# Kernel tuning notes

Hardware: AMD Instinct MI355X
Metric: run time of the kernel (lower is better)

The kernel has to match this reference:

```python
import jax, jax.numpy as jnp
import numpy as np

L, D, H, FF = 6, 768, 12, 3072
DH = D // H
EPS = 1e-12

def _layer_norm(x, g, b):
    mu = jnp.mean(x, axis=-1, keepdims=True)
    var = jnp.mean((x - mu) ** 2, axis=-1, keepdims=True)
    return (x - mu) * jax.lax.rsqrt(var + EPS) * g + b

def setup_inputs() -> dict:
    key = jax.random.key(0)
    ks = jax.random.split(key, 12)
    s = 0.02
    inp = {
        "x": jax.random.normal(ks[0], (8, 512, D), dtype=jnp.float32),
        "attn_mask": jnp.ones((8, 512), dtype=jnp.int32),
        "Wq": jax.random.normal(ks[1], (L, D, D), dtype=jnp.float32) * s,
        "bq": jnp.zeros((L, D), dtype=jnp.float32),
        "Wk": jax.random.normal(ks[2], (L, D, D), dtype=jnp.float32) * s,
        "bk": jnp.zeros((L, D), dtype=jnp.float32),
        "Wv": jax.random.normal(ks[3], (L, D, D), dtype=jnp.float32) * s,
        "bv": jnp.zeros((L, D), dtype=jnp.float32),
        "Wo": jax.random.normal(ks[4], (L, D, D), dtype=jnp.float32) * s,
        "bo": jnp.zeros((L, D), dtype=jnp.float32),
        "ln1_g": jnp.ones((L, D), dtype=jnp.float32),
        "ln1_b": jnp.zeros((L, D), dtype=jnp.float32),
        "W1": jax.random.normal(ks[5], (L, D, FF), dtype=jnp.float32) * s,
        "b1": jnp.zeros((L, FF), dtype=jnp.float32),
        "W2": jax.random.normal(ks[6], (L, FF, D), dtype=jnp.float32) * s,
        "b2": jnp.zeros((L, D), dtype=jnp.float32),
        "ln2_g": jnp.ones((L, D), dtype=jnp.float32),
        "ln2_b": jnp.zeros((L, D), dtype=jnp.float32),
    }
    return inp

def reference(x, attn_mask, Wq, bq, Wk, bk, Wv, bv, Wo, bo,
              ln1_g, ln1_b, W1, b1, W2, b2, ln2_g, ln2_b):
    bs, S, _ = x.shape
    mask_neg = (attn_mask == 0)[:, None, None, :]  # (bs,1,1,S)
    h = x
    for i in range(L):
        def split_heads(t):
            return t.reshape(bs, S, H, DH).transpose(0, 2, 1, 3)  # (bs,H,S,dh)
        q = split_heads(h @ Wq[i] + bq[i]) / jnp.sqrt(jnp.float32(DH))
        k = split_heads(h @ Wk[i] + bk[i])
        v = split_heads(h @ Wv[i] + bv[i])
        scores = jnp.einsum('bhqd,bhkd->bhqk', q, k)
        scores = jnp.where(mask_neg, jnp.float32(-1e9), scores)
        w = jax.nn.softmax(scores, axis=-1)
        ctx = jnp.einsum('bhqk,bhkd->bhqd', w, v)
        ctx = ctx.transpose(0, 2, 1, 3).reshape(bs, S, D)
        sa = ctx @ Wo[i] + bo[i]
        h2 = _layer_norm(sa + h, ln1_g[i], ln1_b[i])
        ffn = jax.nn.gelu(h2 @ W1[i] + b1[i], approximate=False) @ W2[i] + b2[i]
        h = _layer_norm(ffn + h2, ln2_g[i], ln2_b[i])
    return h
```

## Files before the change

kernel.cpp:

```cpp
#include <hip/hip_runtime.h>
#include <math.h>

#define NLAYER 6
#define DMODEL 768
#define NHEAD 12
#define DHEAD 64
#define FFDIM 3072
#define SEQ 512
#define BATCH 8
#define NTOK (BATCH * SEQ)
#define ND ((size_t)NTOK * DMODEL)

typedef __bf16 bf16_t;
typedef __bf16 bf16x8 __attribute__((ext_vector_type(8)));
typedef float f32x4 __attribute__((ext_vector_type(4)));

__device__ __forceinline__ float bf2f(ushort u) {
    return __uint_as_float(((unsigned int)u) << 16);
}
union BFU { __bf16 h; ushort u; };
__device__ __forceinline__ ushort f2b(float x) { BFU c; c.h = (__bf16)x; return c.u; }

#define GLDS(gp, lp) __builtin_amdgcn_global_load_lds( \
    (const __attribute__((address_space(1))) void*)(gp), \
    (__attribute__((address_space(3))) void*)(lp), 16, 0, 0)

__global__ __launch_bounds__(256) void gemm_mfma(
    const ushort* __restrict__ A, const ushort* __restrict__ Bt,
    const float* __restrict__ bias, float* __restrict__ Cf,
    ushort* __restrict__ Cb, int M, int K, int N, int act)
{
    __shared__ __align__(16) ushort As[8192];
    __shared__ __align__(16) ushort Bs[8192];

    const int t = threadIdx.x;
    const int w = t >> 6, l = t & 63;
    const int wr = w >> 1, wc = w & 1;
    const int row0 = blockIdx.y * 128, col0 = blockIdx.x * 128;

    f32x4 acc[4][4];
#pragma unroll
    for (int mi = 0; mi < 4; ++mi)
#pragma unroll
        for (int ni = 0; ni < 4; ++ni)
#pragma unroll
            for (int e = 0; e < 4; ++e) acc[mi][ni][e] = 0.f;

    const int c0 = t,       r0 = c0 >> 2, kg0 = (c0 & 3) ^ ((r0 >> 1) & 3);
    const int c1 = t + 256, r1 = c1 >> 2, kg1 = (c1 & 3) ^ ((r1 >> 1) & 3);
    const ushort* gA0 = A + (size_t)(row0 + r0) * K + kg0 * 8;
    const ushort* gA1 = A + (size_t)(row0 + r1) * K + kg1 * 8;
    const ushort* gB0 = Bt + (size_t)(col0 + r0) * K + kg0 * 8;
    const ushort* gB1 = Bt + (size_t)(col0 + r1) * K + kg1 * 8;

    const int lm = l & 15, lq = l >> 4;
    int aoff[4], boff[4];
#pragma unroll
    for (int mi = 0; mi < 4; ++mi) {
        int m = wr * 64 + mi * 16 + lm;
        aoff[mi] = m * 32 + (lq ^ ((m >> 1) & 3)) * 8;
    }
#pragma unroll
    for (int ni = 0; ni < 4; ++ni) {
        int n = wc * 64 + ni * 16 + lm;
        boff[ni] = n * 32 + (lq ^ ((n >> 1) & 3)) * 8;
    }

#define STAGE_FF(b, k0) do {                                  \
        GLDS(gA0 + (k0), &As[(b) * 4096 + w * 512]);          \
        GLDS(gA1 + (k0), &As[(b) * 4096 + 2048 + w * 512]);   \
        GLDS(gB0 + (k0), &Bs[(b) * 4096 + w * 512]);          \
        GLDS(gB1 + (k0), &Bs[(b) * 4096 + 2048 + w * 512]);   \
    } while (0)

#define COMPUTE_FF(b) do {                                                  \
        bf16x8 af[4], bfr[4];                                               \
        _Pragma("unroll")                                                   \
        for (int mi = 0; mi < 4; ++mi)                                      \
            af[mi] = *(const bf16x8*)&As[(b) * 4096 + aoff[mi]];            \
        _Pragma("unroll")                                                   \
        for (int ni = 0; ni < 4; ++ni)                                      \
            bfr[ni] = *(const bf16x8*)&Bs[(b) * 4096 + boff[ni]];           \
        _Pragma("unroll")                                                   \
        for (int mi = 0; mi < 4; ++mi)                                      \
            _Pragma("unroll")                                               \
            for (int ni = 0; ni < 4; ++ni)                                  \
                acc[mi][ni] = __builtin_amdgcn_mfma_f32_16x16x32_bf16(      \
                    af[mi], bfr[ni], acc[mi][ni], 0, 0, 0);                 \
    } while (0)

    const int nsteps = K >> 5;
    STAGE_FF(0, 0);
    __syncthreads();
    int cur = 0;
    for (int s = 0; s < nsteps - 1; ++s) {
        STAGE_FF(cur ^ 1, (s + 1) * 32);
        COMPUTE_FF(cur);
        __syncthreads();
        cur ^= 1;
    }
    COMPUTE_FF(cur);

#pragma unroll
    for (int mi = 0; mi < 4; ++mi) {
        int rowb = row0 + wr * 64 + mi * 16 + lq * 4;
#pragma unroll
        for (int ni = 0; ni < 4; ++ni) {
            int col = col0 + wc * 64 + ni * 16 + lm;
            float bv = bias[col];
#pragma unroll
            for (int r = 0; r < 4; ++r) {
                float v = acc[mi][ni][r] + bv;
                if (act == 1) v = 0.5f * v * (1.0f + erff(v * 0.70710678118654752f));
                size_t idx = (size_t)(rowb + r) * N + col;
                if (Cb) ((bf16_t*)Cb)[idx] = (bf16_t)v;
                else    Cf[idx] = v;
            }
        }
    }
#undef STAGE_FF
#undef COMPUTE_FF
}

__global__ __launch_bounds__(256) void gemm_mfma_sk(
    const ushort* __restrict__ A, const ushort* __restrict__ Bt,
    const float* __restrict__ bias, float* __restrict__ P0,
    float* __restrict__ P1, int M, int K, int N, int kLen)
{
    __shared__ __align__(16) ushort As[4096];
    __shared__ __align__(16) ushort Bs[8192];

    const int t = threadIdx.x;
    const int w = t >> 6, l = t & 63;
    const int wr = w >> 1, wc = w & 1;
    const int row0 = blockIdx.y * 64, col0 = blockIdx.x * 128;
    const int z = blockIdx.z;
    const int kOff = z * kLen;
    float* Pz = (z == 0) ? P0 : P1;

    f32x4 acc[2][4];
#pragma unroll
    for (int mi = 0; mi < 2; ++mi)
#pragma unroll
        for (int ni = 0; ni < 4; ++ni)
#pragma unroll
            for (int e = 0; e < 4; ++e) acc[mi][ni][e] = 0.f;

    const int rS = t >> 2, kg = (t & 3) ^ ((rS >> 1) & 3);
    const ushort* gA  = A  + (size_t)(row0 + rS) * K + kg * 8;
    const ushort* gB0 = Bt + (size_t)(col0 + rS) * K + kg * 8;
    const ushort* gB1 = Bt + (size_t)(col0 + 64 + rS) * K + kg * 8;

    const int lm = l & 15, lq = l >> 4;
    int aoff[2], boff[4];
#pragma unroll
    for (int mi = 0; mi < 2; ++mi) {
        int m = wr * 32 + mi * 16 + lm;
        aoff[mi] = m * 32 + (lq ^ ((m >> 1) & 3)) * 8;
    }
#pragma unroll
    for (int ni = 0; ni < 4; ++ni) {
        int n = wc * 64 + ni * 16 + lm;
        boff[ni] = n * 32 + (lq ^ ((n >> 1) & 3)) * 8;
    }

#define STAGE_SK(b, k0) do {                                  \
        GLDS(gA  + (k0), &As[(b) * 2048 + w * 512]);          \
        GLDS(gB0 + (k0), &Bs[(b) * 4096 + w * 512]);          \
        GLDS(gB1 + (k0), &Bs[(b) * 4096 + 2048 + w * 512]);   \
    } while (0)

#define COMPUTE_SK(b) do {                                                  \
        bf16x8 af[2], bfr[4];                                               \
        _Pragma("unroll")                                                   \
        for (int mi = 0; mi < 2; ++mi)                                      \
            af[mi] = *(const bf16x8*)&As[(b) * 2048 + aoff[mi]];            \
        _Pragma("unroll")                                                   \
        for (int ni = 0; ni < 4; ++ni)                                      \
            bfr[ni] = *(const bf16x8*)&Bs[(b) * 4096 + boff[ni]];           \
        _Pragma("unroll")                                                   \
        for (int mi = 0; mi < 2; ++mi)                                      \
            _Pragma("unroll")                                               \
            for (int ni = 0; ni < 4; ++ni)                                  \
                acc[mi][ni] = __builtin_amdgcn_mfma_f32_16x16x32_bf16(      \
                    af[mi], bfr[ni], acc[mi][ni], 0, 0, 0);                 \
    } while (0)

    const int nsteps = kLen >> 5;
    STAGE_SK(0, kOff);
    __syncthreads();
    int cur = 0;
    for (int s = 0; s < nsteps - 1; ++s) {
        STAGE_SK(cur ^ 1, kOff + (s + 1) * 32);
        COMPUTE_SK(cur);
        __syncthreads();
        cur ^= 1;
    }
    COMPUTE_SK(cur);

#pragma unroll
    for (int mi = 0; mi < 2; ++mi) {
        int rowb = row0 + wr * 32 + mi * 16 + lq * 4;
#pragma unroll
        for (int ni = 0; ni < 4; ++ni) {
            int col = col0 + wc * 64 + ni * 16 + lm;
            float bv = (z == 0) ? bias[col] : 0.f;
#pragma unroll
            for (int r = 0; r < 4; ++r)
                Pz[(size_t)(rowb + r) * N + col] = acc[mi][ni][r] + bv;
        }
    }
#undef STAGE_SK
#undef COMPUTE_SK
}

__global__ __launch_bounds__(256) void gemm_qkv(
    const ushort* __restrict__ A, const ushort* __restrict__ Bt,
    const float* __restrict__ bq, const float* __restrict__ bk,
    const float* __restrict__ bv,
    ushort* __restrict__ qb, ushort* __restrict__ kb, ushort* __restrict__ vtb)
{
    __shared__ __align__(16) ushort As[4096];
    __shared__ __align__(16) ushort Bs[8192];

    const int K = DMODEL;
    const int t = threadIdx.x;
    const int w = t >> 6, l = t & 63;
    const int wr = w >> 1, wc = w & 1;
    const int row0 = blockIdx.y * 64, col0 = blockIdx.x * 128;
    const int seg = blockIdx.x / 6;

    f32x4 acc[2][4];
#pragma unroll
    for (int mi = 0; mi < 2; ++mi)
#pragma unroll
        for (int ni = 0; ni < 4; ++ni)
#pragma unroll
            for (int e = 0; e < 4; ++e) acc[mi][ni][e] = 0.f;

    const int rS = t >> 2, kg = (t & 3) ^ ((rS >> 1) & 3);
    const ushort* gA  = A  + (size_t)(row0 + rS) * K + kg * 8;
    const ushort* gB0 = Bt + (size_t)(col0 + rS) * K + kg * 8;
    const ushort* gB1 = Bt + (size_t)(col0 + 64 + rS) * K + kg * 8;

    const int lm = l & 15, lq = l >> 4;
    int aoff[2], boff[4];
#pragma unroll
    for (int mi = 0; mi < 2; ++mi) {
        int m = wr * 32 + mi * 16 + lm;
        aoff[mi] = m * 32 + (lq ^ ((m >> 1) & 3)) * 8;
    }
#pragma unroll
    for (int ni = 0; ni < 4; ++ni) {
        int n = wc * 64 + ni * 16 + lm;
        boff[ni] = n * 32 + (lq ^ ((n >> 1) & 3)) * 8;
    }

#define STAGE_QKV(b, k0) do {                                 \
        GLDS(gA  + (k0), &As[(b) * 2048 + w * 512]);          \
        GLDS(gB0 + (k0), &Bs[(b) * 4096 + w * 512]);          \
        GLDS(gB1 + (k0), &Bs[(b) * 4096 + 2048 + w * 512]);   \
    } while (0)

#define COMPUTE_QKV(b) do {                                                 \
        bf16x8 af[2], bfr[4];                                               \
        _Pragma("unroll")                                                   \
        for (int mi = 0; mi < 2; ++mi)                                      \
            af[mi] = *(const bf16x8*)&As[(b) * 2048 + aoff[mi]];            \
        _Pragma("unroll")                                                   \
        for (int ni = 0; ni < 4; ++ni)                                      \
            bfr[ni] = *(const bf16x8*)&Bs[(b) * 4096 + boff[ni]];           \
        _Pragma("unroll")                                                   \
        for (int mi = 0; mi < 2; ++mi)                                      \
            _Pragma("unroll")                                               \
            for (int ni = 0; ni < 4; ++ni)                                  \
                acc[mi][ni] = __builtin_amdgcn_mfma_f32_16x16x32_bf16(      \
                    af[mi], bfr[ni], acc[mi][ni], 0, 0, 0);                 \
    } while (0)

    const int nsteps = K >> 5;
    STAGE_QKV(0, 0);
    __syncthreads();
    int cur = 0;
    for (int s = 0; s < nsteps - 1; ++s) {
        STAGE_QKV(cur ^ 1, (s + 1) * 32);
        COMPUTE_QKV(cur);
        __syncthreads();
        cur ^= 1;
    }
    COMPUTE_QKV(cur);

    const float* bp = (seg == 0) ? bq : (seg == 1) ? bk : bv;
    const float sc = (seg == 0) ? 0.125f : 1.0f;
#pragma unroll
    for (int mi = 0; mi < 2; ++mi) {
        int rowb = row0 + wr * 32 + mi * 16 + lq * 4;
#pragma unroll
        for (int ni = 0; ni < 4; ++ni) {
            int col = col0 + wc * 64 + ni * 16 + lm;
            int lcol = col - seg * 768;
            float bvv = bp[lcol];
            if (seg == 2) {
                int hh = lcol >> 6, dd = lcol & 63;
                int bb = rowb >> 9, ss = rowb & 511;
                ushort4 o;
                o.x = f2b(acc[mi][ni][0] + bvv);
                o.y = f2b(acc[mi][ni][1] + bvv);
                o.z = f2b(acc[mi][ni][2] + bvv);
                o.w = f2b(acc[mi][ni][3] + bvv);
                *(ushort4*)&vtb[(((size_t)(bb * NHEAD + hh)) * DHEAD + dd) * SEQ + ss] = o;
            } else {
                ushort* dst = seg ? kb : qb;
#pragma unroll
                for (int r = 0; r < 4; ++r)
                    dst[(size_t)(rowb + r) * DMODEL + lcol] = f2b((acc[mi][ni][r] + bvv) * sc);
            }
        }
    }
#undef STAGE_QKV
#undef COMPUTE_QKV
}

#define QSTR 72

__global__ __launch_bounds__(256) void attn_mfma(
    const ushort* __restrict__ qb, const ushort* __restrict__ kb,
    const ushort* __restrict__ vtb, const int* __restrict__ mask,
    ushort* __restrict__ ctxb)
{
    __shared__ __align__(16) ushort Qs[64 * QSTR];
    __shared__ __align__(16) ushort Ks[64 * QSTR];
    __shared__ __align__(16) ushort Vs[64 * QSTR];
    __shared__ __align__(16) ushort Ps[64 * QSTR];
    __shared__ float Ma[64];

    const int qt = blockIdx.x, h = blockIdx.y, b = blockIdx.z;
    const int t = threadIdx.x;
    const int w = t >> 6, l = t & 63;
    const int lm = l & 15, lq = l >> 4;

#pragma unroll
    for (int i = 0; i < 2; ++i) {
        int ch = t + i * 256;
        int r = ch >> 3, c8 = ch & 7;
        *(uint4*)&Qs[r * QSTR + c8 * 8] =
            *(const uint4*)&qb[((size_t)(b * SEQ + qt * 64 + r)) * DMODEL + h * DHEAD + c8 * 8];
    }

    f32x4 O[4];
#pragma unroll
    for (int n0 = 0; n0 < 4; ++n0)
#pragma unroll
        for (int e = 0; e < 4; ++e) O[n0][e] = 0.f;
    float mrow[4] = {-3.4e38f, -3.4e38f, -3.4e38f, -3.4e38f};
    float lrow[4] = {0.f, 0.f, 0.f, 0.f};

    const int qrow = w * 16 + lm;
    const int prow = w * 16 + lq * 4;

    for (int kt = 0; kt < SEQ / 64; ++kt) {
#pragma unroll
        for (int i = 0; i < 2; ++i) {
            int ch = t + i * 256;
            int r = ch >> 3, c8 = ch & 7;
            *(uint4*)&Ks[r * QSTR + c8 * 8] =
                *(const uint4*)&kb[((size_t)(b * SEQ + kt * 64 + r)) * DMODEL + h * DHEAD + c8 * 8];
            *(uint4*)&Vs[r * QSTR + c8 * 8] =
                *(const uint4*)&vtb[(((size_t)(b * NHEAD + h)) * DHEAD + r) * SEQ + kt * 64 + c8 * 8];
        }
        if (t < 64) Ma[t] = (mask[b * SEQ + kt * 64 + t] == 0) ? -1e9f : 0.f;
        __syncthreads();

        bf16x8 aq0 = *(const bf16x8*)&Qs[qrow * QSTR + lq * 8];
        bf16x8 aq1 = *(const bf16x8*)&Qs[qrow * QSTR + lq * 8 + 32];
        f32x4 S[4];
#pragma unroll
        for (int n0 = 0; n0 < 4; ++n0) {
#pragma unroll
            for (int e = 0; e < 4; ++e) S[n0][e] = 0.f;
            bf16x8 b0 = *(const bf16x8*)&Ks[(n0 * 16 + lm) * QSTR + lq * 8];
            bf16x8 b1 = *(const bf16x8*)&Ks[(n0 * 16 + lm) * QSTR + lq * 8 + 32];
            S[n0] = __builtin_amdgcn_mfma_f32_16x16x32_bf16(aq0, b0, S[n0], 0, 0, 0);
            S[n0] = __builtin_amdgcn_mfma_f32_16x16x32_bf16(aq1, b1, S[n0], 0, 0, 0);
        }

        float ma4[4];
#pragma unroll
        for (int n0 = 0; n0 < 4; ++n0) ma4[n0] = Ma[n0 * 16 + lm];
#pragma unroll
        for (int n0 = 0; n0 < 4; ++n0)
#pragma unroll
            for (int r = 0; r < 4; ++r) S[n0][r] += ma4[n0];

        float tm[4];
#pragma unroll
        for (int r = 0; r < 4; ++r)
            tm[r] = fmaxf(fmaxf(S[0][r], S[1][r]), fmaxf(S[2][r], S[3][r]));
#pragma unroll
        for (int off = 1; off < 16; off <<= 1)
#pragma unroll
            for (int r = 0; r < 4; ++r)
                tm[r] = fmaxf(tm[r], __shfl_xor(tm[r], off, 64));

        float al[4], ts[4];
#pragma unroll
        for (int r = 0; r < 4; ++r) {
            float mn = fmaxf(mrow[r], tm[r]);
            al[r] = __expf(mrow[r] - mn);
            mrow[r] = mn;
            ts[r] = 0.f;
        }
#pragma unroll
        for (int n0 = 0; n0 < 4; ++n0)
#pragma unroll
            for (int r = 0; r < 4; ++r) {
                float p = __expf(S[n0][r] - mrow[r]);
                ts[r] += p;
                Ps[(prow + r) * QSTR + n0 * 16 + lm] = f2b(p);
            }
#pragma unroll
        for (int off = 1; off < 16; off <<= 1)
#pragma unroll
            for (int r = 0; r < 4; ++r)
                ts[r] += __shfl_xor(ts[r], off, 64);
#pragma unroll
        for (int r = 0; r < 4; ++r) lrow[r] = lrow[r] * al[r] + ts[r];
#pragma unroll
        for (int n0 = 0; n0 < 4; ++n0)
#pragma unroll
            for (int r = 0; r < 4; ++r) O[n0][r] *= al[r];

        bf16x8 ap0 = *(const bf16x8*)&Ps[qrow * QSTR + lq * 8];
        bf16x8 ap1 = *(const bf16x8*)&Ps[qrow * QSTR + lq * 8 + 32];
#pragma unroll
        for (int n0 = 0; n0 < 4; ++n0) {
            bf16x8 v0 = *(const bf16x8*)&Vs[(n0 * 16 + lm) * QSTR + lq * 8];
            bf16x8 v1 = *(const bf16x8*)&Vs[(n0 * 16 + lm) * QSTR + lq * 8 + 32];
            O[n0] = __builtin_amdgcn_mfma_f32_16x16x32_bf16(ap0, v0, O[n0], 0, 0, 0);
            O[n0] = __builtin_amdgcn_mfma_f32_16x16x32_bf16(ap1, v1, O[n0], 0, 0, 0);
        }
        __syncthreads();
    }

    float inv[4];
#pragma unroll
    for (int r = 0; r < 4; ++r) inv[r] = 1.f / lrow[r];
#pragma unroll
    for (int n0 = 0; n0 < 4; ++n0)
#pragma unroll
        for (int r = 0; r < 4; ++r)
            Ks[(prow + r) * QSTR + n0 * 16 + lm] = f2b(O[n0][r] * inv[r]);
    __syncthreads();
#pragma unroll
    for (int i = 0; i < 2; ++i) {
        int ch = t + i * 256;
        int r = ch >> 3, c8 = ch & 7;
        *(uint4*)&ctxb[((size_t)(b * SEQ + qt * 64 + r)) * DMODEL + h * DHEAD + c8 * 8] =
            *(const uint4*)&Ks[r * QSTR + c8 * 8];
    }
}

__global__ __launch_bounds__(256) void transpose_w(
    const float* __restrict__ Wq, const float* __restrict__ Wk,
    const float* __restrict__ Wv, const float* __restrict__ Wo,
    const float* __restrict__ W1, const float* __restrict__ W2,
    ushort* __restrict__ Wqt, ushort* __restrict__ Wkt,
    ushort* __restrict__ Wvt, ushort* __restrict__ Wot,
    ushort* __restrict__ W1t, ushort* __restrict__ W2t)
{
    __shared__ float tile[32][33];
    const int bid = blockIdx.x;
    const float* src; ushort* dst; int K, N, tx, ty;
    if (bid < 2304) {
        int m = bid / 576, tl = bid % 576;
        src = (m == 0) ? Wq : (m == 1) ? Wk : (m == 2) ? Wv : Wo;
        dst = (m == 0) ? Wqt : (m == 1) ? Wkt : (m == 2) ? Wvt : Wot;
        K = 768; N = 768; tx = tl % 24; ty = tl / 24;
    } else if (bid < 4608) {
        int tl = bid - 2304;
        src = W1; dst = W1t; K = 768; N = 3072; tx = tl % 96; ty = tl / 96;
    } else {
        int tl = bid - 4608;
        src = W2; dst = W2t; K = 3072; N = 768; tx = tl % 24; ty = tl / 24;
    }
    const int t = threadIdx.x;
    const int lx = t & 31, ly = t >> 5;
    const int n0 = tx * 32, k0 = ty * 32;
#pragma unroll
    for (int i = 0; i < 4; ++i)
        tile[lx][ly + i * 8] = src[(size_t)(k0 + ly + i * 8) * N + n0 + lx];
    __syncthreads();
#pragma unroll
    for (int i = 0; i < 4; ++i)
        ((bf16_t*)dst)[(size_t)(n0 + ly + i * 8) * K + k0 + lx] =
            (bf16_t)tile[ly + i * 8][lx];
}

__global__ __launch_bounds__(256) void f2bf_kernel(
    const float* __restrict__ src, ushort* __restrict__ dst)
{
    const size_t i = ((size_t)blockIdx.x * 256 + threadIdx.x) * 4;
    float4 v = *(const float4*)(src + i);
    ushort4 o;
    o.x = f2b(v.x); o.y = f2b(v.y); o.z = f2b(v.z); o.w = f2b(v.w);
    *(ushort4*)(dst + i) = o;
}

__global__ __launch_bounds__(256) void add_ln3_kernel(
    const float* __restrict__ p0, const float* __restrict__ p1,
    const float* __restrict__ res,
    const float* __restrict__ gw, const float* __restrict__ bw,
    float* __restrict__ out, ushort* __restrict__ outb)
{
    const int row = blockIdx.x;
    const int t = threadIdx.x;
    __shared__ float red[8];

    const float* a0 = p0 + (size_t)row * DMODEL;
    const float* a1 = p1 + (size_t)row * DMODEL;
    const float* rr = res + (size_t)row * DMODEL;

    float vals[3];
    float s = 0.f;
#pragma unroll
    for (int i = 0; i < 3; ++i) {
        int c = t + i * 256;
        vals[i] = a0[c] + a1[c] + rr[c];
        s += vals[i];
    }
#pragma unroll
    for (int off = 32; off > 0; off >>= 1) s += __shfl_down(s, off, 64);
    if ((t & 63) == 0) red[t >> 6] = s;
    __syncthreads();
    const float mu = (red[0] + red[1] + red[2] + red[3]) * (1.0f / DMODEL);

    float vs = 0.f;
#pragma unroll
    for (int i = 0; i < 3; ++i) {
        float d = vals[i] - mu;
        vs += d * d;
    }
#pragma unroll
    for (int off = 32; off > 0; off >>= 1) vs += __shfl_down(vs, off, 64);
    if ((t & 63) == 0) red[4 + (t >> 6)] = vs;
    __syncthreads();
    const float var = (red[4] + red[5] + red[6] + red[7]) * (1.0f / DMODEL);
    const float inv = rsqrtf(var + 1e-12f);

#pragma unroll
    for (int i = 0; i < 3; ++i) {
        int c = t + i * 256;
        float v = (vals[i] - mu) * inv * gw[c] + bw[c];
        out[(size_t)row * DMODEL + c] = v;
        ((bf16_t*)outb)[(size_t)row * DMODEL + c] = (bf16_t)v;
    }
}

extern "C" void kernel_launch(void* const* d_in, const int* in_sizes, int n_in,
                              void* d_out, int out_size, void* d_ws, size_t ws_size,
                              hipStream_t stream)
{
    const float* x    = (const float*)d_in[0];
    const int*   mask = (const int*)d_in[1];
    const float* Wq = (const float*)d_in[2];
    const float* bq = (const float*)d_in[3];
    const float* Wk = (const float*)d_in[4];
    const float* bk = (const float*)d_in[5];
    const float* Wv = (const float*)d_in[6];
    const float* bv = (const float*)d_in[7];
    const float* Wo = (const float*)d_in[8];
    const float* bo = (const float*)d_in[9];
    const float* ln1g = (const float*)d_in[10];
    const float* ln1b = (const float*)d_in[11];
    const float* W1 = (const float*)d_in[12];
    const float* b1 = (const float*)d_in[13];
    const float* W2 = (const float*)d_in[14];
    const float* b2 = (const float*)d_in[15];
    const float* ln2g = (const float*)d_in[16];
    const float* ln2b = (const float*)d_in[17];

    float* f32b = (float*)d_ws;
    float* hbuf = f32b;
    float* f1   = f32b + ND;
    float* h2   = f32b + 2 * ND;
    ushort* ub  = (ushort*)(f32b + 3 * ND);
    ushort* qb  = ub;
    ushort* kb  = ub + ND;
    ushort* vtb = ub + 2 * ND;
    ushort* hb  = ub + 3 * ND;
    ushort* U   = ub + 4 * ND;
    ushort* ctxb = U;
    ushort* Wqkvt = U + (size_t)NTOK * FFDIM;
    ushort* Wot = Wqkvt + 3 * 768 * 768;
    ushort* W1t = Wot + 768 * 768;
    ushort* W2t = W1t + (size_t)768 * 3072;

    float* p1 = (float*)ub;

    hipMemcpyAsync(hbuf, x, ND * sizeof(float), hipMemcpyDeviceToDevice, stream);
    f2bf_kernel<<<(int)(ND / 1024), 256, 0, stream>>>(x, hb);

    const dim3 gQKV(18, 64);
    const dim3 gSK(6, 64, 2);
    const dim3 gFF(24, 32);
    const dim3 gA(SEQ / 64, NHEAD, BATCH);

    for (int l = 0; l < NLAYER; ++l) {
        const float* Wq_l = Wq + (size_t)l * DMODEL * DMODEL;
        const float* Wk_l = Wk + (size_t)l * DMODEL * DMODEL;
        const float* Wv_l = Wv + (size_t)l * DMODEL * DMODEL;
        const float* Wo_l = Wo + (size_t)l * DMODEL * DMODEL;
        const float* W1_l = W1 + (size_t)l * DMODEL * FFDIM;
        const float* W2_l = W2 + (size_t)l * FFDIM * DMODEL;

        transpose_w<<<6912, 256, 0, stream>>>(Wq_l, Wk_l, Wv_l, Wo_l, W1_l, W2_l,
                                              Wqkvt, Wqkvt + 768 * 768,
                                              Wqkvt + 2 * 768 * 768, Wot, W1t, W2t);

        gemm_qkv<<<gQKV, 256, 0, stream>>>(hb, Wqkvt,
                                           bq + (size_t)l * DMODEL,
                                           bk + (size_t)l * DMODEL,
                                           bv + (size_t)l * DMODEL,
                                           qb, kb, vtb);

        attn_mfma<<<gA, 256, 0, stream>>>(qb, kb, vtb, mask, ctxb);

        gemm_mfma_sk<<<gSK, 256, 0, stream>>>(ctxb, Wot, bo + (size_t)l * DMODEL,
                                              f1, p1, NTOK, DMODEL, DMODEL, DMODEL / 2);

        add_ln3_kernel<<<NTOK, 256, 0, stream>>>(f1, p1, hbuf,
                                                 ln1g + (size_t)l * DMODEL,
                                                 ln1b + (size_t)l * DMODEL, h2, hb);

        gemm_mfma<<<gFF, 256, 0, stream>>>(hb, W1t, b1 + (size_t)l * FFDIM,
                                           nullptr, U, NTOK, DMODEL, FFDIM, 1);

        gemm_mfma_sk<<<gSK, 256, 0, stream>>>(U, W2t, b2 + (size_t)l * DMODEL,
                                              f1, p1, NTOK, FFDIM, DMODEL, FFDIM / 2);

        float* hout = (l == NLAYER - 1) ? (float*)d_out : hbuf;
        add_ln3_kernel<<<NTOK, 256, 0, stream>>>(f1, p1, h2,
                                                 ln2g + (size_t)l * DMODEL,
                                                 ln2b + (size_t)l * DMODEL, hout, hb);
    }
}
```

Measured before the change: 1.284 ms.

## Triple-buffer GEMM LDS staging with vmcnt waits and XCD-aware block swizzle

Converts the three MFMA GEMM kernels from a double-buffered LDS pipeline with __syncthreads to a triple-buffered pipeline. It keeps two K-tiles of global_load_lds in flight and uses explicit s_waitcnt vmcnt counts plus raw s_barrier, so load latency overlaps more compute. It also remaps workgroup IDs with a modulo-8 swizzle so that neighbouring tiles land on the same XCD for better L2 reuse. The cost is 50% more LDS per block, which may reduce occupancy. The hardcoded vmcnt values and swizzle constants depend on exact load counts and grid shapes.

```diff
diff --git a/kernel.cpp b/kernel.cpp
--- a/kernel.cpp
+++ b/kernel.cpp
@@ -30,13 +30,19 @@
     const float* __restrict__ bias, float* __restrict__ Cf,
     ushort* __restrict__ Cb, int M, int K, int N, int act)
 {
-    __shared__ __align__(16) ushort As[8192];
-    __shared__ __align__(16) ushort Bs[8192];
+    __shared__ __align__(16) ushort As[12288];
+    __shared__ __align__(16) ushort Bs[12288];
 
     const int t = threadIdx.x;
     const int w = t >> 6, l = t & 63;
     const int wr = w >> 1, wc = w & 1;
-    const int row0 = blockIdx.y * 128, col0 = blockIdx.x * 128;
+
+    const int hw = blockIdx.x + gridDim.x * blockIdx.y;
+    const int nwg = gridDim.x * gridDim.y;
+    const int sw = (hw & 7) * (nwg >> 3) + (hw >> 3);
+    const int bx = sw % gridDim.x, by = sw / gridDim.x;
+
+    const int row0 = by * 128, col0 = bx * 128;
 
     f32x4 acc[4][4];
 #pragma unroll
@@ -89,17 +95,26 @@
                     af[mi], bfr[ni], acc[mi][ni], 0, 0, 0);                 \
     } while (0)
 
-    const int nsteps = K >> 5;
+    const int nst = K >> 5;
     STAGE_FF(0, 0);
-    __syncthreads();
-    int cur = 0;
-    for (int s = 0; s < nsteps - 1; ++s) {
-        STAGE_FF(cur ^ 1, (s + 1) * 32);
-        COMPUTE_FF(cur);
-        __syncthreads();
-        cur ^= 1;
-    }
-    COMPUTE_FF(cur);
+    STAGE_FF(1, 32);
+    int pb = 2, cb = 0;
+    for (int s = 0; s < nst; ++s) {
+        if (s + 2 < nst) {
+            STAGE_FF(pb, (s + 2) * 32);
+            pb = (pb == 2) ? 0 : pb + 1;
+            asm volatile("s_waitcnt vmcnt(8)" ::: "memory");
+        } else if (s + 2 == nst) {
+            asm volatile("s_waitcnt vmcnt(4)" ::: "memory");
+        } else {
+            asm volatile("s_waitcnt vmcnt(0)" ::: "memory");
+        }
+        __builtin_amdgcn_s_barrier();
+        COMPUTE_FF(cb);
+        asm volatile("s_waitcnt lgkmcnt(0)" ::: "memory");
+        __builtin_amdgcn_s_barrier();
+        cb = (cb == 2) ? 0 : cb + 1;
+    }
 
 #pragma unroll
     for (int mi = 0; mi < 4; ++mi) {
@@ -127,14 +142,20 @@
     const float* __restrict__ bias, float* __restrict__ P0,
     float* __restrict__ P1, int M, int K, int N, int kLen)
 {
-    __shared__ __align__(16) ushort As[4096];
-    __shared__ __align__(16) ushort Bs[8192];
+    __shared__ __align__(16) ushort As[6144];
+    __shared__ __align__(16) ushort Bs[12288];
 
     const int t = threadIdx.x;
     const int w = t >> 6, l = t & 63;
     const int wr = w >> 1, wc = w & 1;
-    const int row0 = blockIdx.y * 64, col0 = blockIdx.x * 128;
-    const int z = blockIdx.z;
+
+    const int hw = blockIdx.x + 6 * blockIdx.y + 384 * blockIdx.z;
+    const int sw = (hw & 7) * 96 + (hw >> 3);
+    const int z  = sw / 384;
+    const int rr_ = sw - z * 384;
+    const int bx = rr_ % 6, by = rr_ / 6;
+
+    const int row0 = by * 64, col0 = bx * 128;
     const int kOff = z * kLen;
     float* Pz = (z == 0) ? P0 : P1;
 
@@ -186,17 +207,26 @@
                     af[mi], bfr[ni], acc[mi][ni], 0, 0, 0);                 \
     } while (0)
 
-    const int nsteps = kLen >> 5;
+    const int nst = kLen >> 5;
     STAGE_SK(0, kOff);
-    __syncthreads();
-    int cur = 0;
-    for (int s = 0; s < nsteps - 1; ++s) {
-        STAGE_SK(cur ^ 1, kOff + (s + 1) * 32);
-        COMPUTE_SK(cur);
-        __syncthreads();
-        cur ^= 1;
-    }
-    COMPUTE_SK(cur);
+    STAGE_SK(1, kOff + 32);
+    int pb = 2, cb = 0;
+    for (int s = 0; s < nst; ++s) {
+        if (s + 2 < nst) {
+            STAGE_SK(pb, kOff + (s + 2) * 32);
+            pb = (pb == 2) ? 0 : pb + 1;
+            asm volatile("s_waitcnt vmcnt(6)" ::: "memory");
+        } else if (s + 2 == nst) {
+            asm volatile("s_waitcnt vmcnt(3)" ::: "memory");
+        } else {
+            asm volatile("s_waitcnt vmcnt(0)" ::: "memory");
+        }
+        __builtin_amdgcn_s_barrier();
+        COMPUTE_SK(cb);
+        asm volatile("s_waitcnt lgkmcnt(0)" ::: "memory");
+        __builtin_amdgcn_s_barrier();
+        cb = (cb == 2) ? 0 : cb + 1;
+    }
 
 #pragma unroll
     for (int mi = 0; mi < 2; ++mi) {
@@ -220,15 +250,20 @@
     const float* __restrict__ bv,
     ushort* __restrict__ qb, ushort* __restrict__ kb, ushort* __restrict__ vtb)
 {
-    __shared__ __align__(16) ushort As[4096];
-    __shared__ __align__(16) ushort Bs[8192];
+    __shared__ __align__(16) ushort As[6144];
+    __shared__ __align__(16) ushort Bs[12288];
 
     const int K = DMODEL;
     const int t = threadIdx.x;
     const int w = t >> 6, l = t & 63;
     const int wr = w >> 1, wc = w & 1;
-    const int row0 = blockIdx.y * 64, col0 = blockIdx.x * 128;
-    const int seg = blockIdx.x / 6;
+
+    const int hw = blockIdx.x + 18 * blockIdx.y;
+    const int sw = (hw & 7) * 144 + (hw >> 3);
+    const int bx = sw % 18, by = sw / 18;
+
+    const int row0 = by * 64, col0 = bx * 128;
+    const int seg = bx / 6;
 
     f32x4 acc[2][4];
 #pragma unroll
@@ -278,17 +313,26 @@
                     af[mi], bfr[ni], acc[mi][ni], 0, 0, 0);                 \
     } while (0)
 
-    const int nsteps = K >> 5;
+    const int nst = K >> 5;
     STAGE_QKV(0, 0);
-    __syncthreads();
-    int cur = 0;
-    for (int s = 0; s < nsteps - 1; ++s) {
-        STAGE_QKV(cur ^ 1, (s + 1) * 32);
-        COMPUTE_QKV(cur);
-        __syncthreads();
-        cur ^= 1;
-    }
-    COMPUTE_QKV(cur);
+    STAGE_QKV(1, 32);
+    int pb = 2, cb = 0;
+    for (int s = 0; s < nst; ++s) {
+        if (s + 2 < nst) {
+            STAGE_QKV(pb, (s + 2) * 32);
+            pb = (pb == 2) ? 0 : pb + 1;
+            asm volatile("s_waitcnt vmcnt(6)" ::: "memory");
+        } else if (s + 2 == nst) {
+            asm volatile("s_waitcnt vmcnt(3)" ::: "memory");
+        } else {
+            asm volatile("s_waitcnt vmcnt(0)" ::: "memory");
+        }
+        __builtin_amdgcn_s_barrier();
+        COMPUTE_QKV(cb);
+        asm volatile("s_waitcnt lgkmcnt(0)" ::: "memory");
+        __builtin_amdgcn_s_barrier();
+        cb = (cb == 2) ? 0 : cb + 1;
+    }
 
     const float* bp = (seg == 0) ? bq : (seg == 1) ? bk : bv;
     const float sc = (seg == 0) ? 0.125f : 1.0f;
```

After: 1.292 ms. No clear change (+0.6%).

## Double K-step per barrier and swizzle workgroup order across XCDs in GEMMs

Applied to the files above, without the earlier changes.

All three GEMM kernels now stage 64 K-elements per pipeline step (two 32-wide sub-tiles) instead of 32, which halves the number of __syncthreads barriers and issues more loads per stage. LDS buffers are doubled to hold this. Workgroup IDs are also remapped so that consecutive tiles land on the same XCD (hw&7 striding), aiming for better L2 locality. The cost is higher LDS use per block, which may lower occupancy, and the swizzle hardcodes grid sizes in the split-K and QKV kernels.

```diff
diff --git a/kernel.cpp b/kernel.cpp
--- a/kernel.cpp
+++ b/kernel.cpp
@@ -30,13 +30,19 @@
     const float* __restrict__ bias, float* __restrict__ Cf,
     ushort* __restrict__ Cb, int M, int K, int N, int act)
 {
-    __shared__ __align__(16) ushort As[8192];
-    __shared__ __align__(16) ushort Bs[8192];
+    __shared__ __align__(16) ushort As[16384];
+    __shared__ __align__(16) ushort Bs[16384];
 
     const int t = threadIdx.x;
     const int w = t >> 6, l = t & 63;
     const int wr = w >> 1, wc = w & 1;
-    const int row0 = blockIdx.y * 128, col0 = blockIdx.x * 128;
+
+    const int hw = blockIdx.x + gridDim.x * blockIdx.y;
+    const int nwg = gridDim.x * gridDim.y;
+    const int sw = (hw & 7) * (nwg >> 3) + (hw >> 3);
+    const int bx = sw % gridDim.x, by = sw / gridDim.x;
+
+    const int row0 = by * 128, col0 = bx * 128;
 
     f32x4 acc[4][4];
 #pragma unroll
@@ -66,35 +72,41 @@
         boff[ni] = n * 32 + (lq ^ ((n >> 1) & 3)) * 8;
     }
 
-#define STAGE_FF(b, k0) do {                                  \
-        GLDS(gA0 + (k0), &As[(b) * 4096 + w * 512]);          \
-        GLDS(gA1 + (k0), &As[(b) * 4096 + 2048 + w * 512]);   \
-        GLDS(gB0 + (k0), &Bs[(b) * 4096 + w * 512]);          \
-        GLDS(gB1 + (k0), &Bs[(b) * 4096 + 2048 + w * 512]);   \
+#define STAGE_FF(b, k0) do {                                              \
+        _Pragma("unroll")                                                 \
+        for (int h = 0; h < 2; ++h) {                                     \
+            GLDS(gA0 + (k0) + h * 32, &As[(b) * 8192 + h * 4096 + w * 512]);        \
+            GLDS(gA1 + (k0) + h * 32, &As[(b) * 8192 + h * 4096 + 2048 + w * 512]); \
+            GLDS(gB0 + (k0) + h * 32, &Bs[(b) * 8192 + h * 4096 + w * 512]);        \
+            GLDS(gB1 + (k0) + h * 32, &Bs[(b) * 8192 + h * 4096 + 2048 + w * 512]); \
+        }                                                                 \
     } while (0)
 
 #define COMPUTE_FF(b) do {                                                  \
-        bf16x8 af[4], bfr[4];                                               \
         _Pragma("unroll")                                                   \
-        for (int mi = 0; mi < 4; ++mi)                                      \
-            af[mi] = *(const bf16x8*)&As[(b) * 4096 + aoff[mi]];            \
-        _Pragma("unroll")                                                   \
-        for (int ni = 0; ni < 4; ++ni)                                      \
-            bfr[ni] = *(const bf16x8*)&Bs[(b) * 4096 + boff[ni]];           \
-        _Pragma("unroll")                                                   \
-        for (int mi = 0; mi < 4; ++mi)                                      \
+        for (int h = 0; h < 2; ++h) {                                       \
+            bf16x8 af[4], bfr[4];                                           \
+            _Pragma("unroll")                                               \
+            for (int mi = 0; mi < 4; ++mi)                                  \
+                af[mi] = *(const bf16x8*)&As[(b) * 8192 + h * 4096 + aoff[mi]]; \
             _Pragma("unroll")                                               \
             for (int ni = 0; ni < 4; ++ni)                                  \
-                acc[mi][ni] = __builtin_amdgcn_mfma_f32_16x16x32_bf16(      \
-                    af[mi], bfr[ni], acc[mi][ni], 0, 0, 0);                 \
+                bfr[ni] = *(const bf16x8*)&Bs[(b) * 8192 + h * 4096 + boff[ni]]; \
+            _Pragma("unroll")                                               \
+            for (int mi = 0; mi < 4; ++mi)                                  \
+                _Pragma("unroll")                                           \
+                for (int ni = 0; ni < 4; ++ni)                              \
+                    acc[mi][ni] = __builtin_amdgcn_mfma_f32_16x16x32_bf16(  \
+                        af[mi], bfr[ni], acc[mi][ni], 0, 0, 0);             \
+        }                                                                   \
     } while (0)
 
-    const int nsteps = K >> 5;
+    const int nst = K >> 6;
     STAGE_FF(0, 0);
     __syncthreads();
     int cur = 0;
-    for (int s = 0; s < nsteps - 1; ++s) {
-        STAGE_FF(cur ^ 1, (s + 1) * 32);
+    for (int s = 0; s < nst - 1; ++s) {
+        STAGE_FF(cur ^ 1, (s + 1) * 64);
         COMPUTE_FF(cur);
         __syncthreads();
         cur ^= 1;
@@ -127,14 +139,20 @@
     const float* __restrict__ bias, float* __restrict__ P0,
     float* __restrict__ P1, int M, int K, int N, int kLen)
 {
-    __shared__ __align__(16) ushort As[4096];
-    __shared__ __align__(16) ushort Bs[8192];
+    __shared__ __align__(16) ushort As[8192];
+    __shared__ __align__(16) ushort Bs[16384];
 
     const int t = threadIdx.x;
     const int w = t >> 6, l = t & 63;
     const int wr = w >> 1, wc = w & 1;
-    const int row0 = blockIdx.y * 64, col0 = blockIdx.x * 128;
-    const int z = blockIdx.z;
+
+    const int hw = blockIdx.x + 6 * blockIdx.y + 384 * blockIdx.z;
+    const int sw = (hw & 7) * 96 + (hw >> 3);
+    const int z  = sw / 384;
+    const int rr_ = sw - z * 384;
+    const int bx = rr_ % 6, by = rr_ / 6;
+
+    const int row0 = by * 64, col0 = bx * 128;
     const int kOff = z * kLen;
     float* Pz = (z == 0) ? P0 : P1;
 
@@ -164,34 +182,40 @@
         boff[ni] = n * 32 + (lq ^ ((n >> 1) & 3)) * 8;
     }
 
-#define STAGE_SK(b, k0) do {                                  \
-        GLDS(gA  + (k0), &As[(b) * 2048 + w * 512]);          \
-        GLDS(gB0 + (k0), &Bs[(b) * 4096 + w * 512]);          \
-        GLDS(gB1 + (k0), &Bs[(b) * 4096 + 2048 + w * 512]);   \
+#define STAGE_SK(b, k0) do {                                              \
+        _Pragma("unroll")                                                 \
+        for (int h = 0; h < 2; ++h) {                                     \
+            GLDS(gA  + (k0) + h * 32, &As[(b) * 4096 + h * 2048 + w * 512]);        \
+            GLDS(gB0 + (k0) + h * 32, &Bs[(b) * 8192 + h * 4096 + w * 512]);        \
+            GLDS(gB1 + (k0) + h * 32, &Bs[(b) * 8192 + h * 4096 + 2048 + w * 512]); \
+        }                                                                 \
     } while (0)
 
 #define COMPUTE_SK(b) do {                                                  \
-        bf16x8 af[2], bfr[4];                                               \
         _Pragma("unroll")                                                   \
-        for (int mi = 0; mi < 2; ++mi)                                      \
-            af[mi] = *(const bf16x8*)&As[(b) * 2048 + aoff[mi]];            \
-        _Pragma("unroll")                                                   \
-        for (int ni = 0; ni < 4; ++ni)                                      \
-            bfr[ni] = *(const bf16x8*)&Bs[(b) * 4096 + boff[ni]];           \
-        _Pragma("unroll")                                                   \
-        for (int mi = 0; mi < 2; ++mi)                                      \
+        for (int h = 0; h < 2; ++h) {                                       \
+            bf16x8 af[2], bfr[4];                                           \
+            _Pragma("unroll")                                               \
+            for (int mi = 0; mi < 2; ++mi)                                  \
+                af[mi] = *(const bf16x8*)&As[(b) * 4096 + h * 2048 + aoff[mi]]; \
             _Pragma("unroll")                                               \
             for (int ni = 0; ni < 4; ++ni)                                  \
-                acc[mi][ni] = __builtin_amdgcn_mfma_f32_16x16x32_bf16(      \
-                    af[mi], bfr[ni], acc[mi][ni], 0, 0, 0);                 \
+                bfr[ni] = *(const bf16x8*)&Bs[(b) * 8192 + h * 4096 + boff[ni]]; \
+            _Pragma("unroll")                                               \
+            for (int mi = 0; mi < 2; ++mi)                                  \
+                _Pragma("unroll")                                           \
+                for (int ni = 0; ni < 4; ++ni)                              \
+                    acc[mi][ni] = __builtin_amdgcn_mfma_f32_16x16x32_bf16(  \
+                        af[mi], bfr[ni], acc[mi][ni], 0, 0, 0);             \
+        }                                                                   \
     } while (0)
 
-    const int nsteps = kLen >> 5;
+    const int nst = kLen >> 6;
     STAGE_SK(0, kOff);
     __syncthreads();
     int cur = 0;
-    for (int s = 0; s < nsteps - 1; ++s) {
-        STAGE_SK(cur ^ 1, kOff + (s + 1) * 32);
+    for (int s = 0; s < nst - 1; ++s) {
+        STAGE_SK(cur ^ 1, kOff + (s + 1) * 64);
         COMPUTE_SK(cur);
         __syncthreads();
         cur ^= 1;
@@ -220,15 +244,20 @@
     const float* __restrict__ bv,
     ushort* __restrict__ qb, ushort* __restrict__ kb, ushort* __restrict__ vtb)
 {
-    __shared__ __align__(16) ushort As[4096];
-    __shared__ __align__(16) ushort Bs[8192];
+    __shared__ __align__(16) ushort As[8192];
+    __shared__ __align__(16) ushort Bs[16384];
 
     const int K = DMODEL;
     const int t = threadIdx.x;
     const int w = t >> 6, l = t & 63;
     const int wr = w >> 1, wc = w & 1;
-    const int row0 = blockIdx.y * 64, col0 = blockIdx.x * 128;
-    const int seg = blockIdx.x / 6;
+
+    const int hw = blockIdx.x + 18 * blockIdx.y;
+    const int sw = (hw & 7) * 144 + (hw >> 3);
+    const int bx = sw % 18, by = sw / 18;
+
+    const int row0 = by * 64, col0 = bx * 128;
+    const int seg = bx / 6;
 
     f32x4 acc[2][4];
 #pragma unroll
@@ -256,34 +285,40 @@
         boff[ni] = n * 32 + (lq ^ ((n >> 1) & 3)) * 8;
     }
 
-#define STAGE_QKV(b, k0) do {                                 \
-        GLDS(gA  + (k0), &As[(b) * 2048 + w * 512]);          \
-        GLDS(gB0 + (k0), &Bs[(b) * 4096 + w * 512]);          \
-        GLDS(gB1 + (k0), &Bs[(b) * 4096 + 2048 + w * 512]);   \
+#define STAGE_QKV(b, k0) do {                                             \
+        _Pragma("unroll")                                                 \
+        for (int h = 0; h < 2; ++h) {                                     \
+            GLDS(gA  + (k0) + h * 32, &As[(b) * 4096 + h * 2048 + w * 512]);        \
+            GLDS(gB0 + (k0) + h * 32, &Bs[(b) * 8192 + h * 4096 + w * 512]);        \
+            GLDS(gB1 + (k0) + h * 32, &Bs[(b) * 8192 + h * 4096 + 2048 + w * 512]); \
+        }                                                                 \
     } while (0)
 
 #define COMPUTE_QKV(b) do {                                                 \
-        bf16x8 af[2], bfr[4];                                               \
         _Pragma("unroll")                                                   \
-        for (int mi = 0; mi < 2; ++mi)                                      \
-            af[mi] = *(const bf16x8*)&As[(b) * 2048 + aoff[mi]];            \
-        _Pragma("unroll")                                                   \
-        for (int ni = 0; ni < 4; ++ni)                                      \
-            bfr[ni] = *(const bf16x8*)&Bs[(b) * 4096 + boff[ni]];           \
-        _Pragma("unroll")                                                   \
-        for (int mi = 0; mi < 2; ++mi)                                      \
+        for (int h = 0; h < 2; ++h) {                                       \
+            bf16x8 af[2], bfr[4];                                           \
+            _Pragma("unroll")                                               \
+            for (int mi = 0; mi < 2; ++mi)                                  \
+                af[mi] = *(const bf16x8*)&As[(b) * 4096 + h * 2048 + aoff[mi]]; \
             _Pragma("unroll")                                               \
             for (int ni = 0; ni < 4; ++ni)                                  \
-                acc[mi][ni] = __builtin_amdgcn_mfma_f32_16x16x32_bf16(      \
-                    af[mi], bfr[ni], acc[mi][ni], 0, 0, 0);                 \
+                bfr[ni] = *(const bf16x8*)&Bs[(b) * 8192 + h * 4096 + boff[ni]]; \
+            _Pragma("unroll")                                               \
+            for (int mi = 0; mi < 2; ++mi)                                  \
+                _Pragma("unroll")                                           \
+                for (int ni = 0; ni < 4; ++ni)                              \
+                    acc[mi][ni] = __builtin_amdgcn_mfma_f32_16x16x32_bf16(  \
+                        af[mi], bfr[ni], acc[mi][ni], 0, 0, 0);             \
+        }                                                                   \
     } while (0)
 
-    const int nsteps = K >> 5;
+    const int nst = K >> 6;
     STAGE_QKV(0, 0);
     __syncthreads();
     int cur = 0;
-    for (int s = 0; s < nsteps - 1; ++s) {
-        STAGE_QKV(cur ^ 1, (s + 1) * 32);
+    for (int s = 0; s < nst - 1; ++s) {
+        STAGE_QKV(cur ^ 1, (s + 1) * 64);
         COMPUTE_QKV(cur);
         __syncthreads();
         cur ^= 1;
```

Result: slower. 1.315 ms (+2.4%).

## Shrink FFN1 tiles, add XCD-aware block swizzle, split FFN2 K four ways

Applied to the files above, without the earlier changes.

The FFN1 GEMM tile drops from 128x128 to 64x128, doubling the grid so more workgroups fill the GPU. All GEMMs remap their block index with an interleave-by-8 swizzle so neighbouring tiles land on the same XCD and share L2. The FFN2 split-K grows from 2 to 4 partials, which a new five-input add+LayerNorm kernel reduces. The extra partials reuse workspace buffers (q/v region and hbuf), which adds memory traffic and relies on those buffers being dead at that point.

```diff
diff --git a/kernel.cpp b/kernel.cpp
--- a/kernel.cpp
+++ b/kernel.cpp
@@ -30,34 +30,38 @@
     const float* __restrict__ bias, float* __restrict__ Cf,
     ushort* __restrict__ Cb, int M, int K, int N, int act)
 {
-    __shared__ __align__(16) ushort As[8192];
+    __shared__ __align__(16) ushort As[4096];
     __shared__ __align__(16) ushort Bs[8192];
 
     const int t = threadIdx.x;
     const int w = t >> 6, l = t & 63;
     const int wr = w >> 1, wc = w & 1;
-    const int row0 = blockIdx.y * 128, col0 = blockIdx.x * 128;
-
-    f32x4 acc[4][4];
-#pragma unroll
-    for (int mi = 0; mi < 4; ++mi)
+
+    const int hw = blockIdx.x + gridDim.x * blockIdx.y;
+    const int nwg = gridDim.x * gridDim.y;
+    const int sw = (hw & 7) * (nwg >> 3) + (hw >> 3);
+    const int bx = sw % gridDim.x, by = sw / gridDim.x;
+
+    const int row0 = by * 64, col0 = bx * 128;
+
+    f32x4 acc[2][4];
+#pragma unroll
+    for (int mi = 0; mi < 2; ++mi)
 #pragma unroll
         for (int ni = 0; ni < 4; ++ni)
 #pragma unroll
             for (int e = 0; e < 4; ++e) acc[mi][ni][e] = 0.f;
 
-    const int c0 = t,       r0 = c0 >> 2, kg0 = (c0 & 3) ^ ((r0 >> 1) & 3);
-    const int c1 = t + 256, r1 = c1 >> 2, kg1 = (c1 & 3) ^ ((r1 >> 1) & 3);
-    const ushort* gA0 = A + (size_t)(row0 + r0) * K + kg0 * 8;
-    const ushort* gA1 = A + (size_t)(row0 + r1) * K + kg1 * 8;
-    const ushort* gB0 = Bt + (size_t)(col0 + r0) * K + kg0 * 8;
-    const ushort* gB1 = Bt + (size_t)(col0 + r1) * K + kg1 * 8;
+    const int rS = t >> 2, kg = (t & 3) ^ ((rS >> 1) & 3);
+    const ushort* gA  = A  + (size_t)(row0 + rS) * K + kg * 8;
+    const ushort* gB0 = Bt + (size_t)(col0 + rS) * K + kg * 8;
+    const ushort* gB1 = Bt + (size_t)(col0 + 64 + rS) * K + kg * 8;
 
     const int lm = l & 15, lq = l >> 4;
-    int aoff[4], boff[4];
-#pragma unroll
-    for (int mi = 0; mi < 4; ++mi) {
-        int m = wr * 64 + mi * 16 + lm;
+    int aoff[2], boff[4];
+#pragma unroll
+    for (int mi = 0; mi < 2; ++mi) {
+        int m = wr * 32 + mi * 16 + lm;
         aoff[mi] = m * 32 + (lq ^ ((m >> 1) & 3)) * 8;
     }
 #pragma unroll
@@ -67,33 +71,32 @@
     }
 
 #define STAGE_FF(b, k0) do {                                  \
-        GLDS(gA0 + (k0), &As[(b) * 4096 + w * 512]);          \
-        GLDS(gA1 + (k0), &As[(b) * 4096 + 2048 + w * 512]);   \
+        GLDS(gA  + (k0), &As[(b) * 2048 + w * 512]);          \
         GLDS(gB0 + (k0), &Bs[(b) * 4096 + w * 512]);          \
         GLDS(gB1 + (k0), &Bs[(b) * 4096 + 2048 + w * 512]);   \
     } while (0)
 
 #define COMPUTE_FF(b) do {                                                  \
-        bf16x8 af[4], bfr[4];                                               \
-        _Pragma("unroll")                                                   \
-        for (int mi = 0; mi < 4; ++mi)                                      \
-            af[mi] = *(const bf16x8*)&As[(b) * 4096 + aoff[mi]];            \
+        bf16x8 af[2], bfr[4];                                               \
+        _Pragma("unroll")                                                   \
+        for (int mi = 0; mi < 2; ++mi)                                      \
+            af[mi] = *(const bf16x8*)&As[(b) * 2048 + aoff[mi]];            \
         _Pragma("unroll")                                                   \
         for (int ni = 0; ni < 4; ++ni)                                      \
             bfr[ni] = *(const bf16x8*)&Bs[(b) * 4096 + boff[ni]];           \
         _Pragma("unroll")                                                   \
-        for (int mi = 0; mi < 4; ++mi)                                      \
+        for (int mi = 0; mi < 2; ++mi)                                      \
             _Pragma("unroll")                                               \
             for (int ni = 0; ni < 4; ++ni)                                  \
                 acc[mi][ni] = __builtin_amdgcn_mfma_f32_16x16x32_bf16(      \
                     af[mi], bfr[ni], acc[mi][ni], 0, 0, 0);                 \
     } while (0)
 
-    const int nsteps = K >> 5;
+    const int nst = K >> 5;
     STAGE_FF(0, 0);
     __syncthreads();
     int cur = 0;
-    for (int s = 0; s < nsteps - 1; ++s) {
+    for (int s = 0; s < nst - 1; ++s) {
         STAGE_FF(cur ^ 1, (s + 1) * 32);
         COMPUTE_FF(cur);
         __syncthreads();
@@ -102,8 +105,8 @@
     COMPUTE_FF(cur);
 
 #pragma unroll
-    for (int mi = 0; mi < 4; ++mi) {
-        int rowb = row0 + wr * 64 + mi * 16 + lq * 4;
+    for (int mi = 0; mi < 2; ++mi) {
+        int rowb = row0 + wr * 32 + mi * 16 + lq * 4;
 #pragma unroll
         for (int ni = 0; ni < 4; ++ni) {
             int col = col0 + wc * 64 + ni * 16 + lm;
@@ -125,7 +128,8 @@
 __global__ __launch_bounds__(256) void gemm_mfma_sk(
     const ushort* __restrict__ A, const ushort* __restrict__ Bt,
     const float* __restrict__ bias, float* __restrict__ P0,
-    float* __restrict__ P1, int M, int K, int N, int kLen)
+    float* __restrict__ P1, float* __restrict__ P2, float* __restrict__ P3,
+    int M, int K, int N, int kLen)
 {
     __shared__ __align__(16) ushort As[4096];
     __shared__ __align__(16) ushort Bs[8192];
@@ -133,10 +137,18 @@
     const int t = threadIdx.x;
     const int w = t >> 6, l = t & 63;
     const int wr = w >> 1, wc = w & 1;
-    const int row0 = blockIdx.y * 64, col0 = blockIdx.x * 128;
-    const int z = blockIdx.z;
+
+    const int X = gridDim.x, XY = gridDim.x * gridDim.y;
+    const int hw = blockIdx.x + X * blockIdx.y + XY * blockIdx.z;
+    const int nwg = XY * gridDim.z;
+    const int sw = (hw & 7) * (nwg >> 3) + (hw >> 3);
+    const int z  = sw / XY;
+    const int rr_ = sw - z * XY;
+    const int bx = rr_ % X, by = rr_ / X;
+
+    const int row0 = by * 64, col0 = bx * 128;
     const int kOff = z * kLen;
-    float* Pz = (z == 0) ? P0 : P1;
+    float* Pz = (z == 0) ? P0 : (z == 1) ? P1 : (z == 2) ? P2 : P3;
 
     f32x4 acc[2][4];
 #pragma unroll
@@ -186,11 +198,11 @@
                     af[mi], bfr[ni], acc[mi][ni], 0, 0, 0);                 \
     } while (0)
 
-    const int nsteps = kLen >> 5;
+    const int nst = kLen >> 5;
     STAGE_SK(0, kOff);
     __syncthreads();
     int cur = 0;
-    for (int s = 0; s < nsteps - 1; ++s) {
+    for (int s = 0; s < nst - 1; ++s) {
         STAGE_SK(cur ^ 1, kOff + (s + 1) * 32);
         COMPUTE_SK(cur);
         __syncthreads();
@@ -227,8 +239,13 @@
     const int t = threadIdx.x;
     const int w = t >> 6, l = t & 63;
     const int wr = w >> 1, wc = w & 1;
-    const int row0 = blockIdx.y * 64, col0 = blockIdx.x * 128;
-    const int seg = blockIdx.x / 6;
+
+    const int hw = blockIdx.x + 18 * blockIdx.y;
+    const int sw = (hw & 7) * 144 + (hw >> 3);
+    const int bx = sw % 18, by = sw / 18;
+
+    const int row0 = by * 64, col0 = bx * 128;
+    const int seg = bx / 6;
 
     f32x4 acc[2][4];
 #pragma unroll
@@ -278,11 +295,11 @@
                     af[mi], bfr[ni], acc[mi][ni], 0, 0, 0);                 \
     } while (0)
 
-    const int nsteps = K >> 5;
+    const int nst = K >> 5;
     STAGE_QKV(0, 0);
     __syncthreads();
     int cur = 0;
-    for (int s = 0; s < nsteps - 1; ++s) {
+    for (int s = 0; s < nst - 1; ++s) {
         STAGE_QKV(cur ^ 1, (s + 1) * 32);
         COMPUTE_QKV(cur);
         __syncthreads();
@@ -526,6 +543,59 @@
     for (int i = 0; i < 3; ++i) {
         int c = t + i * 256;
         vals[i] = a0[c] + a1[c] + rr[c];
+        s += vals[i];
+    }
+#pragma unroll
+    for (int off = 32; off > 0; off >>= 1) s += __shfl_down(s, off, 64);
+    if ((t & 63) == 0) red[t >> 6] = s;
+    __syncthreads();
+    const float mu = (red[0] + red[1] + red[2] + red[3]) * (1.0f / DMODEL);
+
+    float vs = 0.f;
+#pragma unroll
+    for (int i = 0; i < 3; ++i) {
+        float d = vals[i] - mu;
+        vs += d * d;
+    }
+#pragma unroll
+    for (int off = 32; off > 0; off >>= 1) vs += __shfl_down(vs, off, 64);
+    if ((t & 63) == 0) red[4 + (t >> 6)] = vs;
+    __syncthreads();
+    const float var = (red[4] + red[5] + red[6] + red[7]) * (1.0f / DMODEL);
+    const float inv = rsqrtf(var + 1e-12f);
+
+#pragma unroll
+    for (int i = 0; i < 3; ++i) {
+        int c = t + i * 256;
+        float v = (vals[i] - mu) * inv * gw[c] + bw[c];
+        out[(size_t)row * DMODEL + c] = v;
+        ((bf16_t*)outb)[(size_t)row * DMODEL + c] = (bf16_t)v;
+    }
+}
+
+__global__ __launch_bounds__(256) void add_ln5_kernel(
+    const float* __restrict__ p0, const float* __restrict__ p1,
+    const float* __restrict__ p2, const float* __restrict__ p3,
+    const float* __restrict__ res,
+    const float* __restrict__ gw, const float* __restrict__ bw,
+    float* __restrict__ out, ushort* __restrict__ outb)
+{
+    const int row = blockIdx.x;
+    const int t = threadIdx.x;
+    __shared__ float red[8];
+
+    const float* a0 = p0 + (size_t)row * DMODEL;
+    const float* a1 = p1 + (size_t)row * DMODEL;
+    const float* a2 = p2 + (size_t)row * DMODEL;
+    const float* a3 = p3 + (size_t)row * DMODEL;
+    const float* rr = res + (size_t)row * DMODEL;
+
+    float vals[3];
+    float s = 0.f;
+#pragma unroll
+    for (int i = 0; i < 3; ++i) {
+        int c = t + i * 256;
+        vals[i] = (a0[c] + a1[c]) + (a2[c] + a3[c]) + rr[c];
         s += vals[i];
     }
 #pragma unroll
@@ -587,22 +657,26 @@
     ushort* qb  = ub;
     ushort* kb  = ub + ND;
     ushort* vtb = ub + 2 * ND;
-    ushort* hb  = ub + 3 * ND;
+    ushort* hff = ub + 3 * ND;
     ushort* U   = ub + 4 * ND;
     ushort* ctxb = U;
+    ushort* hqkv = U;
     ushort* Wqkvt = U + (size_t)NTOK * FFDIM;
     ushort* Wot = Wqkvt + 3 * 768 * 768;
     ushort* W1t = Wot + 768 * 768;
     ushort* W2t = W1t + (size_t)768 * 3072;
 
     float* p1 = (float*)ub;
+    float* p2 = (float*)(ub + 2 * ND);
+    float* p3 = hbuf;
 
     hipMemcpyAsync(hbuf, x, ND * sizeof(float), hipMemcpyDeviceToDevice, stream);
-    f2bf_kernel<<<(int)(ND / 1024), 256, 0, stream>>>(x, hb);
+    f2bf_kernel<<<(int)(ND / 1024), 256, 0, stream>>>(x, hqkv);
 
     const dim3 gQKV(18, 64);
-    const dim3 gSK(6, 64, 2);
-    const dim3 gFF(24, 32);
+    const dim3 gSKo(6, 64, 2);
+    const dim3 gSK4(6, 64, 4);
+    const dim3 gFF(24, 64);
     const dim3 gA(SEQ / 64, NHEAD, BATCH);
 
     for (int l = 0; l < NLAYER; ++l) {
@@ -617,7 +691,7 @@
                                               Wqkvt, Wqkvt + 768 * 768,
                                               Wqkvt + 2 * 768 * 768, Wot, W1t, W2t);
 
-        gemm_qkv<<<gQKV, 256, 0, stream>>>(hb, Wqkvt,
+        gemm_qkv<<<gQKV, 256, 0, stream>>>(hqkv, Wqkvt,
                                            bq + (size_t)l * DMODEL,
                                            bk + (size_t)l * DMODEL,
                                            bv + (size_t)l * DMODEL,
@@ -625,22 +699,24 @@
 
         attn_mfma<<<gA, 256, 0, stream>>>(qb, kb, vtb, mask, ctxb);
 
-        gemm_mfma_sk<<<gSK, 256, 0, stream>>>(ctxb, Wot, bo + (size_t)l * DMODEL,
-                                              f1, p1, NTOK, DMODEL, DMODEL, DMODEL / 2);
+        gemm_mfma_sk<<<gSKo, 256, 0, stream>>>(ctxb, Wot, bo + (size_t)l * DMODEL,
+                                               f1, p1, p1, p1,
+                                               NTOK, DMODEL, DMODEL, DMODEL / 2);
 
         add_ln3_kernel<<<NTOK, 256, 0, stream>>>(f1, p1, hbuf,
                                                  ln1g + (size_t)l * DMODEL,
-                                                 ln1b + (size_t)l * DMODEL, h2, hb);
-
-        gemm_mfma<<<gFF, 256, 0, stream>>>(hb, W1t, b1 + (size_t)l * FFDIM,
+                                                 ln1b + (size_t)l * DMODEL, h2, hff);
+
+        gemm_mfma<<<gFF, 256, 0, stream>>>(hff, W1t, b1 + (size_t)l * FFDIM,
                                            nullptr, U, NTOK, DMODEL, FFDIM, 1);
 
-        gemm_mfma_sk<<<gSK, 256, 0, stream>>>(U, W2t, b2 + (size_t)l * DMODEL,
-                                              f1, p1, NTOK, FFDIM, DMODEL, FFDIM / 2);
+        gemm_mfma_sk<<<gSK4, 256, 0, stream>>>(U, W2t, b2 + (size_t)l * DMODEL,
+                                               f1, p1, p2, p3,
+                                               NTOK, FFDIM, DMODEL, FFDIM / 4);
 
         float* hout = (l == NLAYER - 1) ? (float*)d_out : hbuf;
-        add_ln3_kernel<<<NTOK, 256, 0, stream>>>(f1, p1, h2,
+        add_ln5_kernel<<<NTOK, 256, 0, stream>>>(f1, p1, p2, p3, h2,
                                                  ln2g + (size_t)l * DMODEL,
-                                                 ln2b + (size_t)l * DMODEL, hout, hb);
-    }
-}
+                                                 ln2b + (size_t)l * DMODEL, hout, hqkv);
+    }
+}
```

Measured after the change: 1.335 ms. +4.0%, slower.
